# Performance work log

Measured on AMD Instinct MI355X. Metric: run time of the kernel, lower is better.

Reference implementation:

```python
import jax, jax.numpy as jnp
import numpy as np
import math

B, C, H, W, M = 8, 256, 128, 128, 7
EPS = 1e-08


def setup_inputs() -> dict:
    key = jax.random.key(0)
    ks = jax.random.split(key, 7)
    x_high = jax.random.normal(ks[0], (B, C, H // 2, W // 2), jnp.float32)
    x_low = jax.random.normal(ks[1], (B, C, H, W), jnp.float32)
    w1 = jax.random.normal(ks[2], (32, M * M), jnp.float32) / np.sqrt(M * M)
    b1 = jnp.zeros((32,), jnp.float32)
    w2 = jax.random.normal(ks[3], (3, 32), jnp.float32) / np.sqrt(32)
    b2 = jnp.zeros((3,), jnp.float32)
    refine_w = jax.random.normal(ks[4], (C, C), jnp.float32) / np.sqrt(C)
    return {"x_high": x_high, "x_low": x_low, "w1": w1, "b1": b1,
            "w2": w2, "b2": b2, "refine_w": refine_w}


def _anisotropic_kernel(params):
    # params: (B,3) -> normalized Gaussian kernels (B, m, m)
    theta = jnp.arctan2(params[:, 0], params[:, 1]) / 2.0 + math.pi / 2.0
    lam1 = jnp.exp(params[:, 2])
    lam2 = 1.0 / (lam1 + EPS)
    coords = jnp.arange(M, dtype=jnp.float32) - (M // 2)  # -3..3
    yy = coords[:, None]  # (m,1) varies along rows (torch meshgrid 'ij')
    xx = coords[None, :]  # (1,m)
    cos_t = jnp.cos(theta)[:, None, None]
    sin_t = jnp.sin(theta)[:, None, None]
    x_rot = xx * cos_t + yy * sin_t          # (B,m,m)
    y_rot = -xx * sin_t + yy * cos_t
    l1 = lam1[:, None, None]
    l2 = lam2[:, None, None]
    k = jnp.exp(-(x_rot ** 2 / (2.0 * l1 ** 2) + y_rot ** 2 / (2.0 * l2 ** 2)))
    return k / (jnp.sum(k, axis=(1, 2), keepdims=True) + EPS)


def _depthwise(x, kern):
    # x: (B,C,H,W), kern: (B,m,m) -> per-sample depthwise conv, kernel shared across C
    k = jnp.repeat(kern, C, axis=0)[:, None, :, :]  # (B*C,1,m,m)
    pad = M // 2
    y = jax.lax.conv_general_dilated(
        x.reshape(1, B * C, H, W), k, (1, 1), [(pad, pad), (pad, pad)],
        dimension_numbers=("NCHW", "OIHW", "NCHW"), feature_group_count=B * C)
    return y.reshape(B, C, H, W)


def reference(x_high, x_low, w1, b1, w2, b2, refine_w):
    # bilinear upsample (align_corners=False == half-pixel, matches jax.image.resize)
    x_high_up = jax.image.resize(x_high, (B, C, H, W), method="bilinear")

    x_f = jnp.fft.fftshift(jnp.fft.fft2(x_low, norm="ortho"), axes=(-2, -1))
    real, imag = jnp.real(x_f), jnp.imag(x_f)
    mag = jnp.abs(x_f)
    mag_weighted = jnp.mean(mag, axis=1, keepdims=True)  # (B,1,H,W)
    h0, w0 = H // 2 - M // 2, W // 2 - M // 2
    mag_center = mag_weighted[:, :, h0:h0 + M, w0:w0 + M]  # (B,1,m,m)

    # param_net: Flatten -> Linear -> ReLU -> Linear
    flat = mag_center.reshape(B, M * M)
    h = jax.nn.relu(flat @ w1.T + b1)
    params = h @ w2.T + b2  # (B,3)

    kern = _anisotropic_kernel(params)
    real_f = _depthwise(real, kern)
    imag_f = _depthwise(imag, kern)

    # 1x1 refine conv (bias-free), shared for real and imag parts
    real_f = jnp.einsum("bchw,oc->bohw", real_f, refine_w)
    imag_f = jnp.einsum("bchw,oc->bohw", imag_f, refine_w)

    out_f = jax.lax.complex(real_f, imag_f)
    out_f = jnp.fft.ifftshift(out_f, axes=(-2, -1))
    x_low_enhanced = jnp.real(jnp.fft.ifft2(out_f, norm="ortho"))
    return x_low_enhanced + x_high_up
```

## Files before the change

kernel.cpp:

```cpp
#include <hip/hip_runtime.h>

typedef __attribute__((ext_vector_type(8))) short bf16x8;
typedef __attribute__((ext_vector_type(4))) float f32x4;
typedef __attribute__((ext_vector_type(4))) int   i32x4;

#define PI_F 3.14159265358979323846f
#define C128 0.0490873852123405f
#define INV_SQRT128 0.0883883476483184f
#define INV128 0.0078125f

#define NB 8
#define NC 256
#define NH 128
#define NW 128
#define IMG 16384
#define NIMG 2048

#define GH_STRIDE 3200
#define AB_STRIDE 3072

__device__ __forceinline__ unsigned short f2bf(float f){
  unsigned int u = __float_as_uint(f);
  u += 0x7FFFu + ((u >> 16) & 1u);
  return (unsigned short)(u >> 16);
}
__device__ __forceinline__ float bf2f(unsigned short u){
  return __uint_as_float(((unsigned int)u) << 16);
}

__device__ __constant__ int c_pcnt[6] = {1,2,3,3,2,1};
__device__ __constant__ int c_pdp0[6] = {6,5,4,0,0,0};

#define COS1 0.9987954562051724f
#define SIN1 0.0490676743274180f
#define K1CH (2.0f*COS1)

#define SM_GG   8320
#define SM_HLR  9344
#define SM_HLI  9856
#define SM_SCRG 1920

__global__ void __launch_bounds__(512, 8) K1(const float* __restrict__ xlow,
                                             float* __restrict__ GH){
  __shared__ float smem[10240];
  unsigned short* xs = (unsigned short*)smem;
  const int tid = threadIdx.x;
  const int img = blockIdx.x;
  float* ghb = GH + (size_t)img*GH_STRIDE;

  {
    const float4* xp = (const float4*)(xlow + (size_t)img*IMG);
    #pragma unroll
    for (int k=0; k<8; ++k){
      int e4 = k*512 + tid;
      float4 v = xp[e4];
      int r = e4 >> 5, c = (e4 & 31)*4;
      unsigned int pw0 = (unsigned int)f2bf(v.x) | ((unsigned int)f2bf(v.y) << 16);
      unsigned int pw1 = (unsigned int)f2bf(v.z) | ((unsigned int)f2bf(v.w) << 16);
      *(unsigned int*)(&xs[r*130 + c    ]) = pw0;
      *(unsigned int*)(&xs[r*130 + c + 2]) = pw1;
    }
  }
  __syncthreads();

  float acc[14];
  #pragma unroll
  for (int i=0;i<14;++i) acc[i]=0.f;

  const int isRow = (tid < 256);
  const int lid  = isRow ? tid : (tid-256);
  const int idx  = lid & 127;
  const int half = lid >> 7;

  {
    const float sg0 = half ? -1.f : 1.f;
    float cp = sg0, sp = 0.f;
    float cn = sg0*COS1, sn = sg0*SIN1;

#define K1_ACCUM(xv, cc, ss)                                   \
    {                                                          \
      float t2 = cc + cc;                                      \
      float c2 = fmaf(t2, cc, -1.f);                           \
      float s2 = t2 * ss;                                      \
      float c3 = fmaf(t2, c2, -cc);                            \
      float s3 = fmaf(t2, s2, -ss);                            \
      acc[0 + PARITY] += xv;                                   \
      acc[2 + PARITY*2]  = fmaf(xv, cc, acc[2 + PARITY*2]);    \
      acc[3 + PARITY*2]  = fmaf(xv, ss, acc[3 + PARITY*2]);    \
      acc[6 + PARITY*2]  = fmaf(xv, c2, acc[6 + PARITY*2]);    \
      acc[7 + PARITY*2]  = fmaf(xv, s2, acc[7 + PARITY*2]);    \
      acc[10 + PARITY*2] = fmaf(xv, c3, acc[10 + PARITY*2]);   \
      acc[11 + PARITY*2] = fmaf(xv, s3, acc[11 + PARITY*2]);   \
    }

    if (isRow){
      const unsigned short* xr = &xs[idx*130 + half*64];
      #pragma unroll 4
      for (int j=0; j<32; ++j){
        unsigned int pk = *(const unsigned int*)(&xr[2*j]);
        float xe = __uint_as_float(pk << 16);
        float xo = __uint_as_float(pk & 0xffff0000u);
#define PARITY 0
        K1_ACCUM(xe, cp, sp)
#undef PARITY
#define PARITY 1
        K1_ACCUM(xo, cn, sn)
#undef PARITY
        float cpn = fmaf(K1CH, cn, -cp);
        float spn = fmaf(K1CH, sn, -sp);
        float cnn = fmaf(K1CH, cpn, -cn);
        float snn = fmaf(K1CH, spn, -sn);
        cp = cpn; sp = spn; cn = cnn; sn = snn;
      }
    } else {
      const unsigned short* xc = &xs[half*64*130 + idx];
      #pragma unroll 4
      for (int j=0; j<32; ++j){
        float xe = bf2f(xc[(2*j  )*130]);
        float xo = bf2f(xc[(2*j+1)*130]);
#define PARITY 0
        K1_ACCUM(xe, cp, sp)
#undef PARITY
#define PARITY 1
        K1_ACCUM(xo, cn, sn)
#undef PARITY
        float cpn = fmaf(K1CH, cn, -cp);
        float spn = fmaf(K1CH, sn, -sp);
        float cnn = fmaf(K1CH, cpn, -cn);
        float snn = fmaf(K1CH, spn, -sn);
        cp = cpn; sp = spn; cn = cnn; sn = snn;
      }
    }
#undef K1_ACCUM
  }
  __syncthreads();

  const int scrbase = (isRow ? 0 : SM_SCRG) + idx*15;
  if (half){
    #pragma unroll
    for (int i=0;i<14;++i) smem[scrbase+i] = acc[i];
  }
  __syncthreads();
  if (!half){
    #pragma unroll
    for (int i=0;i<14;++i) acc[i] += smem[scrbase+i];
    float A0e=acc[0],A0o=acc[1],Ce1=acc[2],Se1=acc[3],Co1=acc[4],So1=acc[5],
          Ce2=acc[6],Se2=acc[7],Co2=acc[8],So2=acc[9],
          Ce3=acc[10],Se3=acc[11],Co3=acc[12],So3=acc[13];
    float d0  = A0e-A0o;
    float dc1 = Ce1-Co1, ds1 = Se1-So1;
    float dc2 = Ce2-Co2, ds2 = Se2-So2;
    float dc3 = Ce3-Co3, ds3 = Se3-So3;
    float* gp = ghb + (isRow ? 1536 : 0);
    const int k = idx;
    gp[(0*2+0)*128+k] = dc3*INV_SQRT128;  gp[(0*2+1)*128+k] =  ds3*INV_SQRT128;
    gp[(1*2+0)*128+k] = dc2*INV_SQRT128;  gp[(1*2+1)*128+k] =  ds2*INV_SQRT128;
    gp[(2*2+0)*128+k] = dc1*INV_SQRT128;  gp[(2*2+1)*128+k] =  ds1*INV_SQRT128;
    gp[(3*2+0)*128+k] = d0 *INV_SQRT128;  gp[(3*2+1)*128+k] =  0.f;
    gp[(4*2+0)*128+k] = dc1*INV_SQRT128;  gp[(4*2+1)*128+k] = -ds1*INV_SQRT128;
    gp[(5*2+0)*128+k] = dc2*INV_SQRT128;  gp[(5*2+1)*128+k] = -ds2*INV_SQRT128;
    if (isRow){
      smem[SM_HLR + 0*128 + k] = A0e+A0o;
      smem[SM_HLR + 1*128 + k] = Ce1+Co1;
      smem[SM_HLR + 2*128 + k] = Ce2+Co2;
      smem[SM_HLR + 3*128 + k] = Ce3+Co3;
      smem[SM_HLI + 0*128 + k] = -(Se1+So1);
      smem[SM_HLI + 1*128 + k] = -(Se2+So2);
      smem[SM_HLI + 2*128 + k] = -(Se3+So3);
    } else {
      smem[SM_GG + (0*2+0)*128 + k] = dc3;  smem[SM_GG + (0*2+1)*128 + k] = ds3;
      smem[SM_GG + (1*2+0)*128 + k] = dc2;  smem[SM_GG + (1*2+1)*128 + k] = ds2;
      smem[SM_GG + (2*2+0)*128 + k] = dc1;  smem[SM_GG + (2*2+1)*128 + k] = ds1;
      smem[SM_GG + (3*2+0)*128 + k] = d0;   smem[SM_GG + (3*2+1)*128 + k] = 0.f;
    }
  }
  __syncthreads();

  if (tid < 144){
    int out = tid >> 2, chunk = tid & 3;
    int wi = out/6, zi = out%6, z = 61+zi;
    int wsrc = (wi<4) ? wi : (wi==4 ? 2 : 1);
    float isg = (wi<4) ? 1.f : -1.f;
    float fR=0.f, fI=0.f;
    const int cEnd = chunk*32 + 32;
    for (int c=chunk*32; c<cEnd; ++c){
      float gR = smem[SM_GG + (wsrc*2  )*128 + c];
      float gI = isg*smem[SM_GG + (wsrc*2+1)*128 + c];
      int m = (z*c) & 127;
      float ts, tc; __sincosf((float)m*C128, &ts, &tc);
      fR += gR*tc + gI*ts;
      fI += gI*tc - gR*ts;
    }
    fR += __shfl_xor(fR,1); fI += __shfl_xor(fI,1);
    fR += __shfl_xor(fR,2); fI += __shfl_xor(fI,2);
    if (chunk==0){
      ghb[3072 + out*2]     = fR * INV128;
      ghb[3072 + out*2 + 1] = fI * INV128;
    }
  }
  if (tid >= 256 && tid < 452){
    int i = (tid-256) >> 2, chunk = (tid-256) & 3;
    int u = i/7 - 3, v = i%7 - 3;
    int va = v < 0 ? -v : v;
    float vsg = v < 0 ? -1.f : 1.f;
    float fR=0.f, fI=0.f;
    const int rEnd = chunk*32 + 32;
    for (int r=chunk*32; r<rEnd; ++r){
      float hR = smem[SM_HLR + va*128 + r];
      float hI = (va==0) ? 0.f : vsg*smem[SM_HLI + (va-1)*128 + r];
      int m = ((u*r) % 128 + 128) & 127;
      float ts, tc; __sincosf((float)m*C128, &ts, &tc);
      fR += hR*tc + hI*ts;
      fI += hI*tc - hR*ts;
    }
    fR += __shfl_xor(fR,1); fI += __shfl_xor(fI,1);
    fR += __shfl_xor(fR,2); fI += __shfl_xor(fI,2);
    if (chunk==0){
      fR *= INV128; fI *= INV128;
      ghb[3144 + i] = sqrtf(fR*fR + fI*fI);
    }
  }
}

__global__ void __launch_bounds__(64) K_mlp(const float* __restrict__ GH,
                                            const float* __restrict__ w1,
                                            const float* __restrict__ b1,
                                            const float* __restrict__ w2,
                                            const float* __restrict__ b2,
                                            float* __restrict__ kern){
  __shared__ float flat[49];
  __shared__ float hh[32];
  const int b = blockIdx.x, tid = threadIdx.x;
  if (tid < 49){
    float s = 0.f;
    for (int c=0; c<256; ++c)
      s += GH[(size_t)(b*256 + c)*GH_STRIDE + 3144 + tid];
    flat[tid] = s * (1.0f/256.0f);
  }
  __syncthreads();
  if (tid < 32){
    float s = b1[tid];
    for (int i=0; i<49; ++i) s += flat[i]*w1[tid*49+i];
    hh[tid] = fmaxf(s, 0.f);
  }
  __syncthreads();
  if (tid == 0){
    float p[3];
    #pragma unroll
    for (int k=0; k<3; ++k){
      float s = b2[k];
      for (int j=0; j<32; ++j) s += hh[j]*w2[k*32+j];
      p[k] = s;
    }
    float theta = atan2f(p[0], p[1])*0.5f + 1.57079632679489662f;
    float ct = cosf(theta), st = sinf(theta);
    float l1 = expf(p[2]);
    float l2 = 1.0f/(l1 + 1e-8f);
    float inv1 = 1.0f/(2.0f*l1*l1);
    float inv2 = 1.0f/(2.0f*l2*l2);
    float sum = 0.f;
    for (int i=0; i<7; ++i) for (int j=0; j<7; ++j){
      float yy = (float)(i-3), xx = (float)(j-3);
      float xr =  xx*ct + yy*st;
      float yr = -xx*st + yy*ct;
      sum += expf(-(xr*xr*inv1 + yr*yr*inv2));
    }
    float inv = 1.0f/(sum + 1e-8f);
    for (int i=0; i<7; ++i) for (int j=0; j<7; ++j){
      float yy = (float)(i-3), xx = (float)(j-3);
      float xr =  xx*ct + yy*st;
      float yr = -xx*st + yy*ct;
      kern[b*49 + i*7 + j] = expf(-(xr*xr*inv1 + yr*yr*inv2)) * inv;
    }
  }
}

__global__ void __launch_bounds__(256) K3(const float* __restrict__ kern,
                                          float* __restrict__ KL,
                                          float* __restrict__ W){
  __shared__ float twc[128], tws[128], kl[49];
  __shared__ float kapl[7][2][128];
  const int b = blockIdx.x, tid = threadIdx.x;
  if (tid < 128){
    float s,c; __sincosf((float)tid*C128, &s, &c);
    twc[tid]=c; tws[tid]=s;
  }
  if (tid < 49) kl[tid] = kern[b*49 + tid];
  __syncthreads();
  if (tid < 128){
    const int c = tid;
    float* klb = KL + (size_t)b*3584;
    #pragma unroll
    for (int dp=0; dp<7; ++dp){
      float kR=0.f, kI=0.f;
      #pragma unroll
      for (int dq=0; dq<7; ++dq){
        int m = (((dq-3)*c) % 128 + 128) & 127;
        float kv = kl[dp*7+dq];
        kR += kv*twc[m]; kI -= kv*tws[m];
      }
      klb[(dp*2  )*128 + c] = kR;
      klb[(dp*2+1)*128 + c] = kI;
      kapl[dp][0][c] = kR; kapl[dp][1][c] = kI;
    }
    const int r = tid;
    #pragma unroll
    for (int dq=0; dq<7; ++dq){
      float lR=0.f, lI=0.f;
      #pragma unroll
      for (int dp=0; dp<7; ++dp){
        int m = (((dp-3)*r) % 128 + 128) & 127;
        float kv = kl[dp*7+dq];
        lR += kv*twc[m]; lI -= kv*tws[m];
      }
      klb[1792 + (dq*2  )*128 + r] = lR;
      klb[1792 + (dq*2+1)*128 + r] = lI;
    }
  }
  __syncthreads();
  for (int k=0;k<64;++k){
    int px = k*256 + tid;
    int r = px >> 7, c = px & 127;
    float w = 0.f;
    #pragma unroll
    for (int dp=0; dp<7; ++dp){
      int m = (((dp-3)*r) % 128 + 128) & 127;
      w += twc[m]*kapl[dp][0][c] + tws[m]*kapl[dp][1][c];
    }
    W[(size_t)b*IMG + px] = w;
  }
}

__global__ void __launch_bounds__(128) K_tab(const float* __restrict__ GH,
                                             const float* __restrict__ KL,
                                             const float* __restrict__ kern,
                                             float* __restrict__ AB){
  __shared__ float dRe[36], dIm[36], kl[49];
  const int tid = threadIdx.x;
  const int img = blockIdx.x, b = img >> 8;
  const float* ghb = GH + (size_t)img*GH_STRIDE;
  const float* klb = KL + (size_t)b*3584;
  float* abb = AB + (size_t)img*AB_STRIDE;

  if (tid < 49) kl[tid] = kern[b*49 + tid];
  __syncthreads();
  if (tid < 36){
    int si = tid/6, ti = tid%6;
    float dR=0.f, dI=0.f;
    for (int j=0; j<c_pcnt[si]; ++j){
      int dp = c_pdp0[si] + j;
      int wi = (si-3) + dp;
      for (int l=0; l<c_pcnt[ti]; ++l){
        int dq = c_pdp0[ti] + l;
        int zi = (ti-3) + dq;
        float kv = kl[dp*7+dq];
        dR += kv * ghb[3072 + (wi*6+zi)*2];
        dI += kv * ghb[3072 + (wi*6+zi)*2 + 1];
      }
    }
    dRe[tid] = dR; dIm[tid] = dI;
  }
  __syncthreads();

  const int c = tid;
  float s1,c1; __sincosf((float)c*C128, &s1, &c1);
  float c2 = c1*c1 - s1*s1, s2 = 2.f*c1*s1;
  float c3 = c1*c2 - s1*s2, s3 = s1*c2 + c1*s2;
  float ct[6] = {c3,c2,c1,1.f,c1,c2};
  float st[6] = {-s3,-s2,-s1,0.f,s1,s2};
  float sgnc = (c & 1) ? -1.f : 1.f;

  float gr[6], gi[6], kr[7], ki[7];
  #pragma unroll
  for (int w=0;w<6;++w){ gr[w]=ghb[(w*2)*128+c]; gi[w]=ghb[(w*2+1)*128+c]; }
  #pragma unroll
  for (int dp=0;dp<7;++dp){ kr[dp]=klb[(dp*2)*128+c]; ki[dp]=klb[(dp*2+1)*128+c]; }

  #pragma unroll
  for (int si=0; si<6; ++si){
    float dR=0.f, dI=0.f;
    for (int j=0; j<c_pcnt[si]; ++j){
      int dp = c_pdp0[si] + j;
      int w = (si-3) + dp;
      dR += kr[dp]*gr[w] - ki[dp]*gi[w];
      dI += kr[dp]*gi[w] + ki[dp]*gr[w];
    }
    float corrR=0.f, corrI=0.f;
    #pragma unroll
    for (int ti=0; ti<6; ++ti){
      float DR = dRe[si*6+ti], DI = dIm[si*6+ti];
      corrR += DR*ct[ti] - DI*st[ti];
      corrI += DR*st[ti] + DI*ct[ti];
    }
    abb[(si*2  )*128 + c] = INV_SQRT128*dR - INV128*sgnc*corrR;
    abb[(si*2+1)*128 + c] = INV_SQRT128*dI - INV128*sgnc*corrI;
  }

  const int r = tid;
  float hr[6], hi_[6], lr[7], li[7];
  #pragma unroll
  for (int z=0;z<6;++z){ hr[z]=ghb[1536+(z*2)*128+r]; hi_[z]=ghb[1536+(z*2+1)*128+r]; }
  #pragma unroll
  for (int dq=0;dq<7;++dq){ lr[dq]=klb[1792+(dq*2)*128+r]; li[dq]=klb[1792+(dq*2+1)*128+r]; }
  #pragma unroll
  for (int ti=0; ti<6; ++ti){
    float bR=0.f, bI=0.f;
    for (int l=0; l<c_pcnt[ti]; ++l){
      int dq = c_pdp0[ti] + l;
      int z = (ti-3) + dq;
      bR += lr[dq]*hr[z] - li[dq]*hi_[z];
      bI += lr[dq]*hi_[z] + li[dq]*hr[z];
    }
    abb[1536 + r*12 + ti*2]     = INV_SQRT128*bR;
    abb[1536 + r*12 + ti*2 + 1] = INV_SQRT128*bI;
  }
}

__global__ void __launch_bounds__(256) K4(const float* __restrict__ xlow,
                                          const float* __restrict__ W,
                                          const float* __restrict__ AB,
                                          unsigned short* __restrict__ filt){
  const int tid = threadIdx.x;
  const int img = blockIdx.x, b = img >> 8;
  const int c0 = (tid & 63)*2, grp = tid >> 6;
  const float* abb = AB + (size_t)img*AB_STRIDE;
  const float* xim = xlow + (size_t)img*IMG;
  const float* Wb  = W + (size_t)b*IMG;
  unsigned short* fim = filt + (size_t)img*IMG;

  float ar[2][6], ai[2][6], ctc[2][6], stc[2][6];
  #pragma unroll
  for (int col=0; col<2; ++col){
    int c = c0 + col;
    #pragma unroll
    for (int si=0;si<6;++si){ ar[col][si]=abb[(si*2)*128+c]; ai[col][si]=abb[(si*2+1)*128+c]; }
    float s1,c1; __sincosf((float)c*C128, &s1, &c1);
    float c2 = c1*c1 - s1*s1, s2 = 2.f*c1*s1;
    float c3 = c1*c2 - s1*s2, s3 = s1*c2 + c1*s2;
    ctc[col][0]=c3; ctc[col][1]=c2; ctc[col][2]=c1; ctc[col][3]=1.f; ctc[col][4]=c1; ctc[col][5]=c2;
    stc[col][0]=-s3; stc[col][1]=-s2; stc[col][2]=-s1; stc[col][3]=0.f; stc[col][4]=s1; stc[col][5]=s2;
  }

  for (int k=0;k<32;++k){
    int ru = __builtin_amdgcn_readfirstlane(grp*32 + k);
    const float* brow = abb + 1536 + ru*12;
    float4 b0 = *(const float4*)(brow);
    float4 b1 = *(const float4*)(brow+4);
    float4 b2 = *(const float4*)(brow+8);
    float rs1,rc1; __sincosf((float)ru*C128, &rs1, &rc1);
    float rc2 = rc1*rc1 - rs1*rs1, rs2 = 2.f*rc1*rs1;
    float rc3 = rc1*rc2 - rs1*rs2, rs3 = rs1*rc2 + rc1*rs2;
    float rcs[6] = {rc3,rc2,rc1,1.f,rc1,rc2};
    float rss[6] = {-rs3,-rs2,-rs1,0.f,rs1,rs2};

    float ER0 = 0.f, ER1 = 0.f;
    #pragma unroll
    for (int si=0;si<6;++si){
      ER0 += rcs[si]*ar[0][si] - rss[si]*ai[0][si];
      ER1 += rcs[si]*ar[1][si] - rss[si]*ai[1][si];
    }
    float rsg = (ru & 1) ? -1.f : 1.f;
    ER0 *= rsg; ER1 *= rsg;

    float bRv[6] = {b0.x, b0.z, b1.x, b1.z, b2.x, b2.z};
    float bIv[6] = {b0.y, b0.w, b1.y, b1.w, b2.y, b2.w};
    float EC0 = 0.f, EC1 = 0.f;
    #pragma unroll
    for (int ti=0;ti<6;++ti){
      EC0 += ctc[0][ti]*bRv[ti] - stc[0][ti]*bIv[ti];
      EC1 += ctc[1][ti]*bRv[ti] - stc[1][ti]*bIv[ti];
    }
    int px = ru*128 + c0;
    float2 xv = *(const float2*)(&xim[px]);
    float2 wv = *(const float2*)(&Wb[px]);
    float v0 = xv.x*wv.x - ER0 - EC0;
    float v1 = xv.y*wv.y - ER1 + EC1;
    unsigned int pack = ((unsigned int)f2bf(v1) << 16) | (unsigned int)f2bf(v0);
    *(unsigned int*)(&fim[px]) = pack;
  }
}

__global__ void __launch_bounds__(256) K_w(const float* __restrict__ rw,
                                           unsigned short* __restrict__ rwbf){
  int i = blockIdx.x*256 + threadIdx.x;
  rwbf[i] = f2bf(rw[i]);
}

__global__ void __launch_bounds__(256) K_up(const float* __restrict__ xhigh,
                                            unsigned short* __restrict__ up){
  __shared__ float xs[64*68];
  const int tid = threadIdx.x;
  const int img = blockIdx.x;
  const float* src = xhigh + (size_t)img*4096;
  unsigned short* dst = up + (size_t)img*IMG;

  #pragma unroll
  for (int p=0; p<4; ++p){
    int t = p*256 + tid;
    float4 v = ((const float4*)src)[t];
    int r = t >> 4, k = t & 15;
    *(float4*)(&xs[r*68 + k*4]) = v;
  }
  __syncthreads();

  for (int k=0; k<32; ++k){
    int pr = k*256 + tid;
    int y = pr >> 6, x0 = (pr & 63)*2;
    float fy = 0.5f*(float)y - 0.25f;
    int iyf = (int)floorf(fy);
    float ty = fy - (float)iyf;
    int iy0 = iyf < 0 ? 0 : iyf;
    int iy1 = (iyf+1) > 63 ? 63 : (iyf+1);
    float wy1 = ty, wy0 = 1.0f - ty;
    const float* r0 = &xs[iy0*68];
    const float* r1 = &xs[iy1*68];

    float outv[2];
    #pragma unroll
    for (int e=0; e<2; ++e){
      int x = x0 + e;
      float fx = 0.5f*(float)x - 0.25f;
      int ixf = (int)floorf(fx);
      float tx = fx - (float)ixf;
      int ix0 = ixf < 0 ? 0 : ixf;
      int ix1 = (ixf+1) > 63 ? 63 : (ixf+1);
      float wx1 = tx, wx0 = 1.0f - tx;
      outv[e] = wy0*(wx0*r0[ix0] + wx1*r0[ix1])
              + wy1*(wx0*r1[ix0] + wx1*r1[ix1]);
    }
    unsigned int pack = ((unsigned int)f2bf(outv[1]) << 16) | (unsigned int)f2bf(outv[0]);
    *(unsigned int*)(&dst[y*NW + x0]) = pack;
  }
}

__global__ void __launch_bounds__(256) K_trans(const unsigned short* __restrict__ in,
                                               unsigned short* __restrict__ outT){
  __shared__ unsigned short tile[64*68];
  const int p0 = blockIdx.x * 64;
  const int c0 = blockIdx.y * 64;
  const int b  = blockIdx.z;
  const int tid = threadIdx.x;
  const int lo = tid >> 4;
  const int q4 = (tid & 15) * 4;

  #pragma unroll
  for (int pass=0; pass<4; ++pass){
    int cc = lo + pass*16;
    ushort4 v = *(const ushort4*)(&in[((size_t)b*NC + c0 + cc)*IMG + p0 + q4]);
    tile[(q4+0)*68 + cc] = v.x;
    tile[(q4+1)*68 + cc] = v.y;
    tile[(q4+2)*68 + cc] = v.z;
    tile[(q4+3)*68 + cc] = v.w;
  }
  __syncthreads();
  #pragma unroll
  for (int pass=0; pass<4; ++pass){
    int pp = lo + pass*16;
    ushort4 v = *(const ushort4*)(&tile[pp*68 + q4]);
    *(ushort4*)(&outT[((size_t)b*IMG + p0 + pp)*NC + c0 + q4]) = v;
  }
}

__global__ void __launch_bounds__(256) K_gemm(const unsigned short* __restrict__ rwbf,
                                              const unsigned short* __restrict__ filtT,
                                              const unsigned short* __restrict__ up,
                                              float* __restrict__ out){
  __shared__ unsigned short At[2][128*32];
  __shared__ unsigned short Bt[2][128*32];
  const int tid = threadIdx.x, lane = tid & 63, wv = tid >> 6;
  const int wr = wv >> 1, wc = wv & 1;
  const int xg = blockIdx.x;
  const int g16 = xg >> 4, i16 = xg & 15;
  const int ot = i16 >> 3, pt = (g16 << 3) | (i16 & 7);
  const int b = blockIdx.z;
  const int p0 = pt*128, o0 = ot*128;

  f32x4 acc[4][4];
  #pragma unroll
  for (int m=0;m<4;++m)
    #pragma unroll
    for (int n=0;n<4;++n){ f32x4 z = {0.f,0.f,0.f,0.f}; acc[m][n] = z; }

  const int row  = tid >> 2;
  const int koff = (tid & 3) * 8;
  const unsigned short* aP0 = &rwbf[(size_t)(o0+row   )*256 + koff];
  const unsigned short* aP1 = &rwbf[(size_t)(o0+row+64)*256 + koff];
  const unsigned short* bP0 = &filtT[((size_t)b*IMG + p0+row   )*256 + koff];
  const unsigned short* bP1 = &filtT[((size_t)b*IMG + p0+row+64)*256 + koff];

  i32x4 av0 = *(const i32x4*)(aP0);
  i32x4 av1 = *(const i32x4*)(aP1);
  i32x4 bv0 = *(const i32x4*)(bP0);
  i32x4 bv1 = *(const i32x4*)(bP1);
  *(i32x4*)(&At[0][ row     *32 + koff]) = av0;
  *(i32x4*)(&At[0][(row+64) *32 + koff]) = av1;
  *(i32x4*)(&Bt[0][ row     *32 + koff]) = bv0;
  *(i32x4*)(&Bt[0][(row+64) *32 + koff]) = bv1;
  __syncthreads();

  const int g = lane >> 4, r16 = lane & 15;
  for (int ks=0; ks<8; ++ks){
    const int cur = ks & 1;
    if (ks < 7){
      const int k0 = (ks+1)*32;
      av0 = *(const i32x4*)(aP0 + k0);
      av1 = *(const i32x4*)(aP1 + k0);
      bv0 = *(const i32x4*)(bP0 + k0);
      bv1 = *(const i32x4*)(bP1 + k0);
    }
    bf16x8 af[4], bfr[4];
    #pragma unroll
    for (int m=0;m<4;++m) af[m]  = *(const bf16x8*)(&At[cur][(wr*64 + m*16 + r16)*32 + g*8]);
    #pragma unroll
    for (int n=0;n<4;++n) bfr[n] = *(const bf16x8*)(&Bt[cur][(wc*64 + n*16 + r16)*32 + g*8]);
    #pragma unroll
    for (int m=0;m<4;++m)
      #pragma unroll
      for (int n=0;n<4;++n)
        acc[m][n] = __builtin_amdgcn_mfma_f32_16x16x32_bf16(af[m], bfr[n], acc[m][n], 0, 0, 0);
    if (ks < 7){
      const int nxt = cur ^ 1;
      *(i32x4*)(&At[nxt][ row     *32 + koff]) = av0;
      *(i32x4*)(&At[nxt][(row+64) *32 + koff]) = av1;
      *(i32x4*)(&Bt[nxt][ row     *32 + koff]) = bv0;
      *(i32x4*)(&Bt[nxt][(row+64) *32 + koff]) = bv1;
      __syncthreads();
    }
  }

  const int y = pt;
  #pragma unroll
  for (int m=0;m<4;++m){
    #pragma unroll
    for (int j=0;j<4;++j){
      int o = o0 + wr*64 + m*16 + g*4 + j;
      size_t base = (size_t)(b*NC + o)*IMG + (size_t)y*NW;
      #pragma unroll
      for (int n=0;n<4;++n){
        int xcol = wc*64 + n*16 + r16;
        float upv = bf2f(up[base + xcol]);
        out[base + xcol] = acc[m][n][j] + upv;
      }
    }
  }
}

extern "C" void kernel_launch(void* const* d_in, const int* in_sizes, int n_in,
                              void* d_out, int out_size, void* d_ws, size_t ws_size,
                              hipStream_t stream){
  (void)in_sizes; (void)n_in; (void)out_size; (void)ws_size;
  const float* xhigh = (const float*)d_in[0];
  const float* xlow  = (const float*)d_in[1];
  const float* w1    = (const float*)d_in[2];
  const float* b1    = (const float*)d_in[3];
  const float* w2    = (const float*)d_in[4];
  const float* b2    = (const float*)d_in[5];
  const float* rw    = (const float*)d_in[6];

  char* ws = (char*)d_ws;
  unsigned short* filt  = (unsigned short*)(ws);
  unsigned short* filtT = (unsigned short*)(ws + 67108864);
  float* GH   = (float*)(ws + 134217728);
  float* AB   = (float*)(ws + 160432128);
  float* kern = (float*)(ws + 185597952);
  float* KL   = (float*)(ws + 185602048);
  float* Wf   = (float*)(ws + 185716736);
  unsigned short* rwbf = (unsigned short*)(ws + 186241024);
  unsigned short* up   = filt;

  K1   <<<NIMG, 512, 0, stream>>>(xlow, GH);
  K_mlp<<<NB,   64,  0, stream>>>(GH, w1, b1, w2, b2, kern);
  K3   <<<NB,   256, 0, stream>>>(kern, KL, Wf);
  K_w  <<<256,  256, 0, stream>>>(rw, rwbf);
  K_tab<<<NIMG, 128, 0, stream>>>(GH, KL, kern, AB);
  K4   <<<NIMG, 256, 0, stream>>>(xlow, Wf, AB, filt);
  K_trans<<<dim3(256, 4, NB), 256, 0, stream>>>(filt, filtT);
  K_up <<<NIMG, 256, 0, stream>>>(xhigh, up);
  K_gemm <<<dim3(256, 1, NB), 256, 0, stream>>>(rwbf, filtT, up, (float*)d_out);
}
```

Baseline: 293.7 us.

## Fuse bilinear upsample into GEMM epilogue and load MFMA operands directly from global

Removes the separate upsample kernel and its bf16 intermediate buffer. The GEMM epilogue now stages the two needed source rows of x_high into shared memory and does the bilinear interpolation itself. The GEMM main loop also drops its LDS double buffer and barriers, loading MFMA fragments straight from global memory into a register double buffer. Separately, two small reduction loops in an earlier kernel rotate their start index per thread to spread shared-memory bank accesses. The trade-off is global loads that are less coalesced (16-byte strided per lane) and more register pressure.

```diff
diff --git a/kernel.cpp b/kernel.cpp
--- a/kernel.cpp
+++ b/kernel.cpp
@@ -182,8 +182,8 @@
     int wsrc = (wi<4) ? wi : (wi==4 ? 2 : 1);
     float isg = (wi<4) ? 1.f : -1.f;
     float fR=0.f, fI=0.f;
-    const int cEnd = chunk*32 + 32;
-    for (int c=chunk*32; c<cEnd; ++c){
+    for (int ii=0; ii<32; ++ii){
+      int c = chunk*32 + ((ii + tid) & 31);
       float gR = smem[SM_GG + (wsrc*2  )*128 + c];
       float gI = isg*smem[SM_GG + (wsrc*2+1)*128 + c];
       int m = (z*c) & 127;
@@ -204,8 +204,8 @@
     int va = v < 0 ? -v : v;
     float vsg = v < 0 ? -1.f : 1.f;
     float fR=0.f, fI=0.f;
-    const int rEnd = chunk*32 + 32;
-    for (int r=chunk*32; r<rEnd; ++r){
+    for (int ii=0; ii<32; ++ii){
+      int r = chunk*32 + ((ii + tid) & 31);
       float hR = smem[SM_HLR + va*128 + r];
       float hI = (va==0) ? 0.f : vsg*smem[SM_HLI + (va-1)*128 + r];
       int m = ((u*r) % 128 + 128) & 127;
@@ -486,53 +486,6 @@
   rwbf[i] = f2bf(rw[i]);
 }
 
-__global__ void __launch_bounds__(256) K_up(const float* __restrict__ xhigh,
-                                            unsigned short* __restrict__ up){
-  __shared__ float xs[64*68];
-  const int tid = threadIdx.x;
-  const int img = blockIdx.x;
-  const float* src = xhigh + (size_t)img*4096;
-  unsigned short* dst = up + (size_t)img*IMG;
-
-  #pragma unroll
-  for (int p=0; p<4; ++p){
-    int t = p*256 + tid;
-    float4 v = ((const float4*)src)[t];
-    int r = t >> 4, k = t & 15;
-    *(float4*)(&xs[r*68 + k*4]) = v;
-  }
-  __syncthreads();
-
-  for (int k=0; k<32; ++k){
-    int pr = k*256 + tid;
-    int y = pr >> 6, x0 = (pr & 63)*2;
-    float fy = 0.5f*(float)y - 0.25f;
-    int iyf = (int)floorf(fy);
-    float ty = fy - (float)iyf;
-    int iy0 = iyf < 0 ? 0 : iyf;
-    int iy1 = (iyf+1) > 63 ? 63 : (iyf+1);
-    float wy1 = ty, wy0 = 1.0f - ty;
-    const float* r0 = &xs[iy0*68];
-    const float* r1 = &xs[iy1*68];
-
-    float outv[2];
-    #pragma unroll
-    for (int e=0; e<2; ++e){
-      int x = x0 + e;
-      float fx = 0.5f*(float)x - 0.25f;
-      int ixf = (int)floorf(fx);
-      float tx = fx - (float)ixf;
-      int ix0 = ixf < 0 ? 0 : ixf;
-      int ix1 = (ixf+1) > 63 ? 63 : (ixf+1);
-      float wx1 = tx, wx0 = 1.0f - tx;
-      outv[e] = wy0*(wx0*r0[ix0] + wx1*r0[ix1])
-              + wy1*(wx0*r1[ix0] + wx1*r1[ix1]);
-    }
-    unsigned int pack = ((unsigned int)f2bf(outv[1]) << 16) | (unsigned int)f2bf(outv[0]);
-    *(unsigned int*)(&dst[y*NW + x0]) = pack;
-  }
-}
-
 __global__ void __launch_bounds__(256) K_trans(const unsigned short* __restrict__ in,
                                                unsigned short* __restrict__ outT){
   __shared__ unsigned short tile[64*68];
@@ -563,10 +516,9 @@
 
 __global__ void __launch_bounds__(256) K_gemm(const unsigned short* __restrict__ rwbf,
                                               const unsigned short* __restrict__ filtT,
-                                              const unsigned short* __restrict__ up,
+                                              const float* __restrict__ xhigh,
                                               float* __restrict__ out){
-  __shared__ unsigned short At[2][128*32];
-  __shared__ unsigned short Bt[2][128*32];
+  __shared__ unsigned short epi[128*132];
   const int tid = threadIdx.x, lane = tid & 63, wv = tid >> 6;
   const int wr = wv >> 1, wc = wv & 1;
   const int xg = blockIdx.x;
@@ -574,6 +526,14 @@
   const int ot = i16 >> 3, pt = (g16 << 3) | (i16 & 7);
   const int b = blockIdx.z;
   const int p0 = pt*128, o0 = ot*128;
+  const int g = lane >> 4, r16 = lane & 15;
+
+  const unsigned short* aBase[4];
+  const unsigned short* bBase[4];
+  #pragma unroll
+  for (int m=0;m<4;++m) aBase[m] = &rwbf[(size_t)(o0 + wr*64 + m*16 + r16)*256 + g*8];
+  #pragma unroll
+  for (int n=0;n<4;++n) bBase[n] = &filtT[((size_t)b*IMG + p0 + wc*64 + n*16 + r16)*256 + g*8];
 
   f32x4 acc[4][4];
   #pragma unroll
@@ -581,65 +541,75 @@
     #pragma unroll
     for (int n=0;n<4;++n){ f32x4 z = {0.f,0.f,0.f,0.f}; acc[m][n] = z; }
 
-  const int row  = tid >> 2;
-  const int koff = (tid & 3) * 8;
-  const unsigned short* aP0 = &rwbf[(size_t)(o0+row   )*256 + koff];
-  const unsigned short* aP1 = &rwbf[(size_t)(o0+row+64)*256 + koff];
-  const unsigned short* bP0 = &filtT[((size_t)b*IMG + p0+row   )*256 + koff];
-  const unsigned short* bP1 = &filtT[((size_t)b*IMG + p0+row+64)*256 + koff];
-
-  i32x4 av0 = *(const i32x4*)(aP0);
-  i32x4 av1 = *(const i32x4*)(aP1);
-  i32x4 bv0 = *(const i32x4*)(bP0);
-  i32x4 bv1 = *(const i32x4*)(bP1);
-  *(i32x4*)(&At[0][ row     *32 + koff]) = av0;
-  *(i32x4*)(&At[0][(row+64) *32 + koff]) = av1;
-  *(i32x4*)(&Bt[0][ row     *32 + koff]) = bv0;
-  *(i32x4*)(&Bt[0][(row+64) *32 + koff]) = bv1;
-  __syncthreads();
-
-  const int g = lane >> 4, r16 = lane & 15;
+  bf16x8 aReg[2][4], bReg[2][4];
+  #pragma unroll
+  for (int m=0;m<4;++m) aReg[0][m] = *(const bf16x8*)(aBase[m]);
+  #pragma unroll
+  for (int n=0;n<4;++n) bReg[0][n] = *(const bf16x8*)(bBase[n]);
+
+  #pragma unroll
   for (int ks=0; ks<8; ++ks){
-    const int cur = ks & 1;
+    const int cur = ks & 1, nxt = cur ^ 1;
     if (ks < 7){
-      const int k0 = (ks+1)*32;
-      av0 = *(const i32x4*)(aP0 + k0);
-      av1 = *(const i32x4*)(aP1 + k0);
-      bv0 = *(const i32x4*)(bP0 + k0);
-      bv1 = *(const i32x4*)(bP1 + k0);
-    }
-    bf16x8 af[4], bfr[4];
-    #pragma unroll
-    for (int m=0;m<4;++m) af[m]  = *(const bf16x8*)(&At[cur][(wr*64 + m*16 + r16)*32 + g*8]);
-    #pragma unroll
-    for (int n=0;n<4;++n) bfr[n] = *(const bf16x8*)(&Bt[cur][(wc*64 + n*16 + r16)*32 + g*8]);
+      #pragma unroll
+      for (int m=0;m<4;++m) aReg[nxt][m] = *(const bf16x8*)(aBase[m] + (ks+1)*32);
+      #pragma unroll
+      for (int n=0;n<4;++n) bReg[nxt][n] = *(const bf16x8*)(bBase[n] + (ks+1)*32);
+    }
     #pragma unroll
     for (int m=0;m<4;++m)
       #pragma unroll
       for (int n=0;n<4;++n)
-        acc[m][n] = __builtin_amdgcn_mfma_f32_16x16x32_bf16(af[m], bfr[n], acc[m][n], 0, 0, 0);
-    if (ks < 7){
-      const int nxt = cur ^ 1;
-      *(i32x4*)(&At[nxt][ row     *32 + koff]) = av0;
-      *(i32x4*)(&At[nxt][(row+64) *32 + koff]) = av1;
-      *(i32x4*)(&Bt[nxt][ row     *32 + koff]) = bv0;
-      *(i32x4*)(&Bt[nxt][(row+64) *32 + koff]) = bv1;
-      __syncthreads();
-    }
+        acc[m][n] = __builtin_amdgcn_mfma_f32_16x16x32_bf16(aReg[cur][m], bReg[cur][n], acc[m][n], 0, 0, 0);
   }
 
   const int y = pt;
-  #pragma unroll
-  for (int m=0;m<4;++m){
-    #pragma unroll
-    for (int j=0;j<4;++j){
-      int o = o0 + wr*64 + m*16 + g*4 + j;
-      size_t base = (size_t)(b*NC + o)*IMG + (size_t)y*NW;
+  float fy = 0.5f*(float)y - 0.25f;
+  int iyf = (int)floorf(fy);
+  float ty = fy - (float)iyf;
+  int iy0 = iyf < 0 ? 0 : iyf;
+  int iy1 = (iyf+1) > 63 ? 63 : (iyf+1);
+  float wy1 = ty, wy0 = 1.0f - ty;
+
+  {
+    int ol = tid >> 1, half = tid & 1;
+    const float* s0 = &xhigh[((size_t)(b*NC + o0 + ol)*64 + iy0)*64 + half*32];
+    const float* s1 = &xhigh[((size_t)(b*NC + o0 + ol)*64 + iy1)*64 + half*32];
+    unsigned short* d0 = &epi[ol*132 + half*32];
+    unsigned short* d1 = &epi[ol*132 + 64 + half*32];
+    #pragma unroll
+    for (int i=0;i<8;++i){
+      float4 v0 = *(const float4*)(s0 + i*4);
+      float4 v1 = *(const float4*)(s1 + i*4);
+      *(unsigned int*)(&d0[i*4  ]) = (unsigned int)f2bf(v0.x) | ((unsigned int)f2bf(v0.y) << 16);
+      *(unsigned int*)(&d0[i*4+2]) = (unsigned int)f2bf(v0.z) | ((unsigned int)f2bf(v0.w) << 16);
+      *(unsigned int*)(&d1[i*4  ]) = (unsigned int)f2bf(v1.x) | ((unsigned int)f2bf(v1.y) << 16);
+      *(unsigned int*)(&d1[i*4+2]) = (unsigned int)f2bf(v1.z) | ((unsigned int)f2bf(v1.w) << 16);
+    }
+  }
+  __syncthreads();
+
+  #pragma unroll
+  for (int n=0;n<4;++n){
+    int xcol = wc*64 + n*16 + r16;
+    float fx = 0.5f*(float)xcol - 0.25f;
+    int ixf = (int)floorf(fx);
+    float tx = fx - (float)ixf;
+    int ix0 = ixf < 0 ? 0 : ixf;
+    int ix1 = (ixf+1) > 63 ? 63 : (ixf+1);
+    float wx1 = tx, wx0 = 1.0f - tx;
+    #pragma unroll
+    for (int m=0;m<4;++m){
       #pragma unroll
-      for (int n=0;n<4;++n){
-        int xcol = wc*64 + n*16 + r16;
-        float upv = bf2f(up[base + xcol]);
-        out[base + xcol] = acc[m][n][j] + upv;
+      for (int j=0;j<4;++j){
+        int olo = wr*64 + m*16 + g*4 + j;
+        float v00 = bf2f(epi[olo*132 + ix0]);
+        float v01 = bf2f(epi[olo*132 + ix1]);
+        float v10 = bf2f(epi[olo*132 + 64 + ix0]);
+        float v11 = bf2f(epi[olo*132 + 64 + ix1]);
+        float up = wy0*(wx0*v00 + wx1*v01) + wy1*(wx0*v10 + wx1*v11);
+        int o = o0 + olo;
+        out[((size_t)(b*NC + o))*IMG + (size_t)y*NW + xcol] = acc[m][n][j] + up;
       }
     }
   }
@@ -666,7 +636,6 @@
   float* KL   = (float*)(ws + 185602048);
   float* Wf   = (float*)(ws + 185716736);
   unsigned short* rwbf = (unsigned short*)(ws + 186241024);
-  unsigned short* up   = filt;
 
   K1   <<<NIMG, 512, 0, stream>>>(xlow, GH);
   K_mlp<<<NB,   64,  0, stream>>>(GH, w1, b1, w2, b2, kern);
@@ -675,6 +644,5 @@
   K_tab<<<NIMG, 128, 0, stream>>>(GH, KL, kern, AB);
   K4   <<<NIMG, 256, 0, stream>>>(xlow, Wf, AB, filt);
   K_trans<<<dim3(256, 4, NB), 256, 0, stream>>>(filt, filtT);
-  K_up <<<NIMG, 256, 0, stream>>>(xhigh, up);
-  K_gemm <<<dim3(256, 1, NB), 256, 0, stream>>>(rwbf, filtT, up, (float*)d_out);
-}
+  K_gemm <<<dim3(256, 1, NB), 256, 0, stream>>>(rwbf, filtT, xhigh, (float*)d_out);
+}
```

Result: slower. 341.6 us (+16.3%).

## Fuse channel transpose into GEMM B-tile load and drop the transpose kernel

Applied to the files above, without the earlier changes.

Removes the separate K_trans kernel that rewrote the filtered bf16 tensor into pixel-major layout. The GEMM now reads the channel-major filt tensor directly and transposes it in registers while storing into shared memory, whose rows are padded to 40 to limit bank conflicts. This saves a full read and write of a 64 MB intermediate plus one launch. In exchange, B-tile global loads now stride across channel planes, and the shared-memory stores become scattered 32-bit writes. The upsample buffer moves to its own workspace region because filt is no longer free to reuse.

```diff
diff --git a/kernel.cpp b/kernel.cpp
--- a/kernel.cpp
+++ b/kernel.cpp
@@ -533,40 +533,12 @@
   }
 }
 
-__global__ void __launch_bounds__(256) K_trans(const unsigned short* __restrict__ in,
-                                               unsigned short* __restrict__ outT){
-  __shared__ unsigned short tile[64*68];
-  const int p0 = blockIdx.x * 64;
-  const int c0 = blockIdx.y * 64;
-  const int b  = blockIdx.z;
-  const int tid = threadIdx.x;
-  const int lo = tid >> 4;
-  const int q4 = (tid & 15) * 4;
-
-  #pragma unroll
-  for (int pass=0; pass<4; ++pass){
-    int cc = lo + pass*16;
-    ushort4 v = *(const ushort4*)(&in[((size_t)b*NC + c0 + cc)*IMG + p0 + q4]);
-    tile[(q4+0)*68 + cc] = v.x;
-    tile[(q4+1)*68 + cc] = v.y;
-    tile[(q4+2)*68 + cc] = v.z;
-    tile[(q4+3)*68 + cc] = v.w;
-  }
-  __syncthreads();
-  #pragma unroll
-  for (int pass=0; pass<4; ++pass){
-    int pp = lo + pass*16;
-    ushort4 v = *(const ushort4*)(&tile[pp*68 + q4]);
-    *(ushort4*)(&outT[((size_t)b*IMG + p0 + pp)*NC + c0 + q4]) = v;
-  }
-}
-
 __global__ void __launch_bounds__(256) K_gemm(const unsigned short* __restrict__ rwbf,
-                                              const unsigned short* __restrict__ filtT,
+                                              const unsigned short* __restrict__ filt,
                                               const unsigned short* __restrict__ up,
                                               float* __restrict__ out){
-  __shared__ unsigned short At[2][128*32];
-  __shared__ unsigned short Bt[2][128*32];
+  __shared__ unsigned short At[2][128*40];
+  __shared__ unsigned short Bt[2][128*40];
   const int tid = threadIdx.x, lane = tid & 63, wv = tid >> 6;
   const int wr = wv >> 1, wc = wv & 1;
   const int xg = blockIdx.x;
@@ -581,38 +553,54 @@
     #pragma unroll
     for (int n=0;n<4;++n){ f32x4 z = {0.f,0.f,0.f,0.f}; acc[m][n] = z; }
 
-  const int row  = tid >> 2;
-  const int koff = (tid & 3) * 8;
-  const unsigned short* aP0 = &rwbf[(size_t)(o0+row   )*256 + koff];
-  const unsigned short* aP1 = &rwbf[(size_t)(o0+row+64)*256 + koff];
-  const unsigned short* bP0 = &filtT[((size_t)b*IMG + p0+row   )*256 + koff];
-  const unsigned short* bP1 = &filtT[((size_t)b*IMG + p0+row+64)*256 + koff];
+  const int arow  = tid >> 2;
+  const int akoff = (tid & 3) * 8;
+  const unsigned short* aP0 = &rwbf[(size_t)(o0+arow   )*256 + akoff];
+  const unsigned short* aP1 = &rwbf[(size_t)(o0+arow+64)*256 + akoff];
+
+  const int bc2 = (tid & 15) * 2;
+  const int bpo = (tid >> 4) * 8;
+  const unsigned short* bP0 = &filt[((size_t)b*NC + bc2    )*IMG + p0 + bpo];
+  const unsigned short* bP1 = &filt[((size_t)b*NC + bc2 + 1)*IMG + p0 + bpo];
 
   i32x4 av0 = *(const i32x4*)(aP0);
   i32x4 av1 = *(const i32x4*)(aP1);
   i32x4 bv0 = *(const i32x4*)(bP0);
   i32x4 bv1 = *(const i32x4*)(bP1);
-  *(i32x4*)(&At[0][ row     *32 + koff]) = av0;
-  *(i32x4*)(&At[0][(row+64) *32 + koff]) = av1;
-  *(i32x4*)(&Bt[0][ row     *32 + koff]) = bv0;
-  *(i32x4*)(&Bt[0][(row+64) *32 + koff]) = bv1;
+
+#define BT_STORE(BUF)                                                        \
+  {                                                                          \
+    _Pragma("unroll")                                                        \
+    for (int j=0;j<4;++j){                                                   \
+      unsigned int w0 = (unsigned int)bv0[j];                                \
+      unsigned int w1 = (unsigned int)bv1[j];                                \
+      unsigned int lo = (w0 & 0xffffu) | (w1 << 16);                         \
+      unsigned int hi = (w0 >> 16) | (w1 & 0xffff0000u);                     \
+      *(unsigned int*)(&Bt[BUF][(bpo+2*j  )*40 + bc2]) = lo;                 \
+      *(unsigned int*)(&Bt[BUF][(bpo+2*j+1)*40 + bc2]) = hi;                 \
+    }                                                                        \
+  }
+
+  *(i32x4*)(&At[0][ arow    *40 + akoff]) = av0;
+  *(i32x4*)(&At[0][(arow+64)*40 + akoff]) = av1;
+  BT_STORE(0)
   __syncthreads();
 
   const int g = lane >> 4, r16 = lane & 15;
   for (int ks=0; ks<8; ++ks){
     const int cur = ks & 1;
     if (ks < 7){
-      const int k0 = (ks+1)*32;
-      av0 = *(const i32x4*)(aP0 + k0);
-      av1 = *(const i32x4*)(aP1 + k0);
-      bv0 = *(const i32x4*)(bP0 + k0);
-      bv1 = *(const i32x4*)(bP1 + k0);
+      const int ka = (ks+1)*32;
+      av0 = *(const i32x4*)(aP0 + ka);
+      av1 = *(const i32x4*)(aP1 + ka);
+      bv0 = *(const i32x4*)(bP0 + (size_t)(ks+1)*32*IMG);
+      bv1 = *(const i32x4*)(bP1 + (size_t)(ks+1)*32*IMG);
     }
     bf16x8 af[4], bfr[4];
     #pragma unroll
-    for (int m=0;m<4;++m) af[m]  = *(const bf16x8*)(&At[cur][(wr*64 + m*16 + r16)*32 + g*8]);
-    #pragma unroll
-    for (int n=0;n<4;++n) bfr[n] = *(const bf16x8*)(&Bt[cur][(wc*64 + n*16 + r16)*32 + g*8]);
+    for (int m=0;m<4;++m) af[m]  = *(const bf16x8*)(&At[cur][(wr*64 + m*16 + r16)*40 + g*8]);
+    #pragma unroll
+    for (int n=0;n<4;++n) bfr[n] = *(const bf16x8*)(&Bt[cur][(wc*64 + n*16 + r16)*40 + g*8]);
     #pragma unroll
     for (int m=0;m<4;++m)
       #pragma unroll
@@ -620,13 +608,13 @@
         acc[m][n] = __builtin_amdgcn_mfma_f32_16x16x32_bf16(af[m], bfr[n], acc[m][n], 0, 0, 0);
     if (ks < 7){
       const int nxt = cur ^ 1;
-      *(i32x4*)(&At[nxt][ row     *32 + koff]) = av0;
-      *(i32x4*)(&At[nxt][(row+64) *32 + koff]) = av1;
-      *(i32x4*)(&Bt[nxt][ row     *32 + koff]) = bv0;
-      *(i32x4*)(&Bt[nxt][(row+64) *32 + koff]) = bv1;
+      *(i32x4*)(&At[nxt][ arow    *40 + akoff]) = av0;
+      *(i32x4*)(&At[nxt][(arow+64)*40 + akoff]) = av1;
+      if (nxt) BT_STORE(1) else BT_STORE(0)
       __syncthreads();
     }
   }
+#undef BT_STORE
 
   const int y = pt;
   #pragma unroll
@@ -659,14 +647,13 @@
 
   char* ws = (char*)d_ws;
   unsigned short* filt  = (unsigned short*)(ws);
-  unsigned short* filtT = (unsigned short*)(ws + 67108864);
+  unsigned short* up    = (unsigned short*)(ws + 67108864);
   float* GH   = (float*)(ws + 134217728);
   float* AB   = (float*)(ws + 160432128);
   float* kern = (float*)(ws + 185597952);
   float* KL   = (float*)(ws + 185602048);
   float* Wf   = (float*)(ws + 185716736);
   unsigned short* rwbf = (unsigned short*)(ws + 186241024);
-  unsigned short* up   = filt;
 
   K1   <<<NIMG, 512, 0, stream>>>(xlow, GH);
   K_mlp<<<NB,   64,  0, stream>>>(GH, w1, b1, w2, b2, kern);
@@ -674,7 +661,6 @@
   K_w  <<<256,  256, 0, stream>>>(rw, rwbf);
   K_tab<<<NIMG, 128, 0, stream>>>(GH, KL, kern, AB);
   K4   <<<NIMG, 256, 0, stream>>>(xlow, Wf, AB, filt);
-  K_trans<<<dim3(256, 4, NB), 256, 0, stream>>>(filt, filtT);
   K_up <<<NIMG, 256, 0, stream>>>(xhigh, up);
-  K_gemm <<<dim3(256, 1, NB), 256, 0, stream>>>(rwbf, filtT, up, (float*)d_out);
-}
+  K_gemm <<<dim3(256, 1, NB), 256, 0, stream>>>(rwbf, filt, up, (float*)d_out);
+}
```

After: 301.1 us. +2.5%, slower.
